# Kernel tuning notes

Measured on AMD Instinct MI355X. Metric: run time of the kernel, lower is better.

The kernel has to match this reference:

```python
import jax, jax.numpy as jnp
import numpy as np

EMBED_DIM = 512
N_HEADS = 8
HEAD_DIM = EMBED_DIM // N_HEADS


def setup_inputs() -> dict:
    key = jax.random.key(0)
    ks = jax.random.split(key, 8)
    B, S, D = 8, 2048, EMBED_DIM
    scale = 1.0 / np.sqrt(D)
    return {
        "key": jax.random.normal(ks[0], (B, S, D), dtype=jnp.float32),
        "query": jax.random.normal(ks[1], (B, S, D), dtype=jnp.float32),
        "value": jax.random.normal(ks[2], (B, S, D), dtype=jnp.float32),
        # nn.Linear stores weight as [out, in]; y = x @ W.T. We store W_T=[in,out].
        "Wq": jax.random.normal(ks[3], (D, D), dtype=jnp.float32) * scale,
        "Wk": jax.random.normal(ks[4], (D, D), dtype=jnp.float32) * scale,
        "Wv": jax.random.normal(ks[5], (D, D), dtype=jnp.float32) * scale,
        "Wo": jax.random.normal(ks[6], (D, D), dtype=jnp.float32) * scale,
        "bo": jax.random.normal(ks[7], (D,), dtype=jnp.float32) * scale,
    }


def reference(key, query, value, Wq, Wk, Wv, Wo, bo):
    B, S, D = key.shape
    Sq = query.shape[1]
    H, Hd = N_HEADS, HEAD_DIM
    # projections (no bias for q/k/v)
    q = (query @ Wq).reshape(B, Sq, H, Hd)
    k = (key @ Wk).reshape(B, S, H, Hd)
    v = (value @ Wv).reshape(B, S, H, Hd)
    # scores: [B, H, Sq, S]
    product = jnp.einsum("bqhd,bkhd->bhqk", q, k) / np.sqrt(Hd)
    scores = jax.nn.softmax(product, axis=-1)
    out = jnp.einsum("bhqk,bkhd->bqhd", scores, v).reshape(B, Sq, D)
    return out @ Wo + bo
```

## Files before the change

### kernel.cpp

```cpp
#include <hip/hip_runtime.h>

typedef _Float16 half8 __attribute__((ext_vector_type(8)));
typedef _Float16 half4 __attribute__((ext_vector_type(4)));
typedef __fp16 fp16x2 __attribute__((ext_vector_type(2)));
typedef float floatx16 __attribute__((ext_vector_type(16)));
typedef unsigned int uint2v __attribute__((ext_vector_type(2)));

#define MFMA_F16 __builtin_amdgcn_mfma_f32_32x32x16_f16

__device__ __forceinline__ float fast_exp2(float x) {
#if __has_builtin(__builtin_amdgcn_exp2f)
    return __builtin_amdgcn_exp2f(x);
#else
    return exp2f(x);
#endif
}

__device__ __forceinline__ half4 pack4(float a, float b, float c, float d) {
    union { fp16x2 p[2]; half4 h; } u;
    u.p[0] = __builtin_amdgcn_cvt_pkrtz(a, b);
    u.p[1] = __builtin_amdgcn_cvt_pkrtz(c, d);
    return u.h;
}

__device__ __forceinline__ unsigned int pk2(float a, float b) {
    union { fp16x2 p; unsigned int u; } v;
    v.p = __builtin_amdgcn_cvt_pkrtz(a, b);
    return v.u;
}

__device__ __forceinline__ half8 ld_frag_lds(const _Float16* p) {
    union { half8 v; half4 h[2]; } u;
    u.h[0] = *(const half4*)(p);
    u.h[1] = *(const half4*)(p + 4);
    return u.v;
}

__device__ __forceinline__ void tile_barrier() {
    asm volatile("s_waitcnt lgkmcnt(0)" ::: "memory");
    __builtin_amdgcn_s_barrier();
    asm volatile("" ::: "memory");
}

__device__ __forceinline__ half8 pv_frag(const unsigned int* w, int i0) {
    uint2v s0 = __builtin_amdgcn_permlane32_swap(w[2 * i0 + 0], w[2 * i0 + 2], false, false);
    uint2v s1 = __builtin_amdgcn_permlane32_swap(w[2 * i0 + 1], w[2 * i0 + 3], false, false);
    union { unsigned int u[4]; half8 h; } pu;
    pu.u[0] = s0[0];
    pu.u[1] = s1[0];
    pu.u[2] = s0[1];
    pu.u[3] = s1[1];
    return pu.h;
}

__global__ __launch_bounds__(256) void wcvt_kernel(const float* __restrict__ Wq,
                                                   const float* __restrict__ Wk,
                                                   const float* __restrict__ Wv,
                                                   const float* __restrict__ Wo,
                                                   _Float16* __restrict__ Wt) {
    __shared__ _Float16 T[64 * 68];
    const int bx   = blockIdx.x;
    const int wsel = bx >> 6;
    const int tile = bx & 63;
    const int to   = (tile >> 3) * 64;
    const int ti   = (tile & 7) * 64;
    const float* src = (wsel == 0) ? Wq : (wsel == 1) ? Wk : (wsel == 2) ? Wv : Wo;
    const int t = threadIdx.x;
    const int rloc = t >> 4, c4 = (t & 15) * 4;
#pragma unroll
    for (int m = 0; m < 4; m++) {
        int i = ti + rloc + 16 * m;
        float4 f = *(const float4*)(src + (size_t)i * 512 + to + c4);
        T[(c4 + 0) * 68 + rloc + 16 * m] = (_Float16)f.x;
        T[(c4 + 1) * 68 + rloc + 16 * m] = (_Float16)f.y;
        T[(c4 + 2) * 68 + rloc + 16 * m] = (_Float16)f.z;
        T[(c4 + 3) * 68 + rloc + 16 * m] = (_Float16)f.w;
    }
    __syncthreads();
    const int o_loc = t >> 2, ich = (t & 3) * 16;
    const _Float16* s = &T[o_loc * 68 + ich];
    _Float16* dst = Wt + (size_t)wsel * 262144 + (size_t)(to + o_loc) * 512 + ti + ich;
    half4 a0 = *(const half4*)(s);
    half4 a1 = *(const half4*)(s + 4);
    half4 a2 = *(const half4*)(s + 8);
    half4 a3 = *(const half4*)(s + 12);
    *(half4*)(dst)      = a0;
    *(half4*)(dst + 4)  = a1;
    *(half4*)(dst + 8)  = a2;
    *(half4*)(dst + 12) = a3;
}

__global__ __launch_bounds__(256, 3) void qkv_gemm(const float* __restrict__ query,
                                                   const float* __restrict__ key,
                                                   const float* __restrict__ value,
                                                   const _Float16* __restrict__ Wt,
                                                   _Float16* __restrict__ Qh,
                                                   _Float16* __restrict__ Kh,
                                                   _Float16* __restrict__ Vt,
                                                   float C1) {
    __shared__ _Float16 Alds[128 * 68];
    __shared__ _Float16 Blds[128 * 68];

    const int z = blockIdx.z;
    const float* A = (z == 0) ? query : (z == 1) ? key : value;
    const _Float16* W = Wt + (size_t)z * 262144;

    const int tid  = threadIdx.x;
    const int lane = tid & 63;
    const int w    = tid >> 6;
    const int l31  = lane & 31;
    const int lh   = lane >> 5;
    const int wm   = w >> 1;
    const int wn   = w & 1;
    const int n0   = blockIdx.x * 128;
    const int m0   = blockIdx.y * 128;
    const int crow = tid >> 3;
    const int ck8  = (tid & 7) * 8;

    floatx16 acc[2][2];
#pragma unroll
    for (int i = 0; i < 2; i++)
#pragma unroll
        for (int j = 0; j < 2; j++)
#pragma unroll
            for (int r = 0; r < 16; r++) acc[i][j][r] = 0.0f;

    float4 apre[4][2];
    int4   bpre[4];
#pragma unroll
    for (int i = 0; i < 4; i++) {
        const float* p = A + (size_t)(m0 + crow + 32 * i) * 512 + ck8;
        apre[i][0] = *(const float4*)(p);
        apre[i][1] = *(const float4*)(p + 4);
        bpre[i] = *(const int4*)(W + (size_t)(n0 + crow + 32 * i) * 512 + ck8);
    }

    for (int t = 0; t < 8; t++) {
        __syncthreads();
#pragma unroll
        for (int i = 0; i < 4; i++) {
            int r = crow + 32 * i;
            float4 f0 = apre[i][0], f1 = apre[i][1];
            *(half4*)&Alds[r * 68 + ck8]     = pack4(f0.x, f0.y, f0.z, f0.w);
            *(half4*)&Alds[r * 68 + ck8 + 4] = pack4(f1.x, f1.y, f1.z, f1.w);
            *(int2*)&Blds[r * 68 + ck8]      = make_int2(bpre[i].x, bpre[i].y);
            *(int2*)&Blds[r * 68 + ck8 + 4]  = make_int2(bpre[i].z, bpre[i].w);
        }
        __syncthreads();
        if (t < 7) {
            int ks2 = (t + 1) * 64;
#pragma unroll
            for (int i = 0; i < 4; i++) {
                const float* p = A + (size_t)(m0 + crow + 32 * i) * 512 + ks2 + ck8;
                apre[i][0] = *(const float4*)(p);
                apre[i][1] = *(const float4*)(p + 4);
                bpre[i] = *(const int4*)(W + (size_t)(n0 + crow + 32 * i) * 512 + ks2 + ck8);
            }
        }
#pragma unroll
        for (int kc = 0; kc < 4; kc++) {
            int kb = kc * 16 + lh * 8;
            half8 af[2], bf[2];
            af[0] = ld_frag_lds(&Alds[(wm * 64 + l31) * 68 + kb]);
            af[1] = ld_frag_lds(&Alds[(wm * 64 + 32 + l31) * 68 + kb]);
            bf[0] = ld_frag_lds(&Blds[(wn * 64 + l31) * 68 + kb]);
            bf[1] = ld_frag_lds(&Blds[(wn * 64 + 32 + l31) * 68 + kb]);
#pragma unroll
            for (int i = 0; i < 2; i++)
#pragma unroll
                for (int j = 0; j < 2; j++)
                    acc[i][j] = MFMA_F16(af[i], bf[j], acc[i][j], 0, 0, 0);
        }
    }

    const float oscale = (z == 0) ? C1 : 1.0f;
    _Float16* out01 = (z == 0) ? Qh : Kh;
#pragma unroll
    for (int i = 0; i < 2; i++) {
#pragma unroll
        for (int j = 0; j < 2; j++) {
            int gn    = n0 + wn * 64 + j * 32 + l31;
            int mbase = m0 + wm * 64 + i * 32 + 4 * lh;
            int h = gn >> 6, hd = gn & 63;
            if (z < 2) {
#pragma unroll
                for (int r = 0; r < 16; r++) {
                    int gm = mbase + (r & 3) + 8 * (r >> 2);
                    int b = gm >> 11, s = gm & 2047;
                    out01[(size_t)((b * 8 + h) * 2048 + s) * 64 + hd] =
                        (_Float16)(acc[i][j][r] * oscale);
                }
            } else {
#pragma unroll
                for (int g = 0; g < 4; g++) {
                    int gm = mbase + 8 * g;
                    int b = gm >> 11, s = gm & 2047;
                    *(half4*)&Vt[(size_t)((b * 8 + h) * 64 + hd) * 2048 + s] =
                        pack4(acc[i][j][4 * g + 0], acc[i][j][4 * g + 1],
                              acc[i][j][4 * g + 2], acc[i][j][4 * g + 3]);
                }
            }
        }
    }
}

__global__ __launch_bounds__(256, 3) void out_gemm(const _Float16* __restrict__ A,
                                                   const _Float16* __restrict__ W,
                                                   const float* __restrict__ bias,
                                                   float* __restrict__ out) {
    __shared__ _Float16 Alds[128 * 68];
    __shared__ _Float16 Blds[128 * 68];

    const int tid  = threadIdx.x;
    const int lane = tid & 63;
    const int w    = tid >> 6;
    const int l31  = lane & 31;
    const int lh   = lane >> 5;
    const int wm   = w >> 1;
    const int wn   = w & 1;
    const int n0   = blockIdx.x * 128;
    const int m0   = blockIdx.y * 128;
    const int crow = tid >> 3;
    const int ck8  = (tid & 7) * 8;

    floatx16 acc[2][2];
#pragma unroll
    for (int i = 0; i < 2; i++)
#pragma unroll
        for (int j = 0; j < 2; j++)
#pragma unroll
            for (int r = 0; r < 16; r++) acc[i][j][r] = 0.0f;

    int4 apre[4], bpre[4];
#pragma unroll
    for (int i = 0; i < 4; i++) {
        apre[i] = *(const int4*)(A + (size_t)(m0 + crow + 32 * i) * 512 + ck8);
        bpre[i] = *(const int4*)(W + (size_t)(n0 + crow + 32 * i) * 512 + ck8);
    }

    for (int t = 0; t < 8; t++) {
        __syncthreads();
#pragma unroll
        for (int i = 0; i < 4; i++) {
            int r = crow + 32 * i;
            *(int2*)&Alds[r * 68 + ck8]     = make_int2(apre[i].x, apre[i].y);
            *(int2*)&Alds[r * 68 + ck8 + 4] = make_int2(apre[i].z, apre[i].w);
            *(int2*)&Blds[r * 68 + ck8]     = make_int2(bpre[i].x, bpre[i].y);
            *(int2*)&Blds[r * 68 + ck8 + 4] = make_int2(bpre[i].z, bpre[i].w);
        }
        __syncthreads();
        if (t < 7) {
            int ks2 = (t + 1) * 64;
#pragma unroll
            for (int i = 0; i < 4; i++) {
                apre[i] = *(const int4*)(A + (size_t)(m0 + crow + 32 * i) * 512 + ks2 + ck8);
                bpre[i] = *(const int4*)(W + (size_t)(n0 + crow + 32 * i) * 512 + ks2 + ck8);
            }
        }
#pragma unroll
        for (int kc = 0; kc < 4; kc++) {
            int kb = kc * 16 + lh * 8;
            half8 af[2], bf[2];
            af[0] = ld_frag_lds(&Alds[(wm * 64 + l31) * 68 + kb]);
            af[1] = ld_frag_lds(&Alds[(wm * 64 + 32 + l31) * 68 + kb]);
            bf[0] = ld_frag_lds(&Blds[(wn * 64 + l31) * 68 + kb]);
            bf[1] = ld_frag_lds(&Blds[(wn * 64 + 32 + l31) * 68 + kb]);
#pragma unroll
            for (int i = 0; i < 2; i++)
#pragma unroll
                for (int j = 0; j < 2; j++)
                    acc[i][j] = MFMA_F16(af[i], bf[j], acc[i][j], 0, 0, 0);
        }
    }

#pragma unroll
    for (int i = 0; i < 2; i++) {
#pragma unroll
        for (int j = 0; j < 2; j++) {
            int gn    = n0 + wn * 64 + j * 32 + l31;
            int mbase = m0 + wm * 64 + i * 32 + 4 * lh;
            float bv = bias[gn];
#pragma unroll
            for (int r = 0; r < 16; r++) {
                int gm = mbase + (r & 3) + 8 * (r >> 2);
                out[(size_t)gm * 512 + gn] = acc[i][j][r] + bv;
            }
        }
    }
}

__global__ __launch_bounds__(256, 3) void attn_kernel(const _Float16* __restrict__ Qg,
                                                      const _Float16* __restrict__ Kg,
                                                      const _Float16* __restrict__ Vg,
                                                      _Float16* __restrict__ AO) {
    __shared__ _Float16 Kbuf[2][64 * 68];

    const int tid  = threadIdx.x;
    const int lane = tid & 63;
    const int w    = tid >> 6;
    const int l31  = lane & 31;
    const int lh   = lane >> 5;
    const int h    = blockIdx.y;
    const int b    = blockIdx.z;
    const int q0   = blockIdx.x * 128 + w * 32;

    const size_t bhoff = (size_t)(b * 8 + h) * (2048 * 64);
    const _Float16* Qbh = Qg + bhoff;
    const _Float16* Kbh = Kg + bhoff;
    const _Float16* Vbh = Vg + bhoff;

    const _Float16* Vrow0 = Vbh + (size_t)l31 * 2048 + lh * 8;
    const _Float16* Vrow1 = Vbh + (size_t)(32 + l31) * 2048 + lh * 8;

    const int c0row = tid >> 3, ck8 = (tid & 7) * 8;
    const int c1row = c0row + 32;

    half8 qf[4];
#pragma unroll
    for (int kc = 0; kc < 4; kc++)
        qf[kc] = *(const half8*)(Qbh + (size_t)(q0 + l31) * 64 + kc * 16 + lh * 8);

    floatx16 O[2];
#pragma unroll
    for (int i = 0; i < 2; i++)
#pragma unroll
        for (int r = 0; r < 16; r++) O[i][r] = 0.0f;
    float lsum = 0.0f;

    unsigned int w16[16];
    half8 vf[4][2];

    int4 kpre[2];
    kpre[0] = *(const int4*)(Kbh + c0row * 64 + ck8);
    kpre[1] = *(const int4*)(Kbh + c1row * 64 + ck8);
    *(int2*)&Kbuf[0][c0row * 68 + ck8]     = make_int2(kpre[0].x, kpre[0].y);
    *(int2*)&Kbuf[0][c0row * 68 + ck8 + 4] = make_int2(kpre[0].z, kpre[0].w);
    *(int2*)&Kbuf[0][c1row * 68 + ck8]     = make_int2(kpre[1].x, kpre[1].y);
    *(int2*)&Kbuf[0][c1row * 68 + ck8 + 4] = make_int2(kpre[1].z, kpre[1].w);
    kpre[0] = *(const int4*)(Kbh + 4096 + c0row * 64 + ck8);
    kpre[1] = *(const int4*)(Kbh + 4096 + c1row * 64 + ck8);
    tile_barrier();

    for (int kt = 0; kt < 32; kt++) {
        const int cur = kt & 1;
        const _Float16* Kc = Kbuf[cur];

#pragma unroll
        for (int kc = 0; kc < 4; kc++) {
            vf[kc][0] = *(const half8*)(Vrow0 + kt * 64 + kc * 16);
            vf[kc][1] = *(const half8*)(Vrow1 + kt * 64 + kc * 16);
        }

        if (kt < 31) {
            _Float16* Kd = Kbuf[cur ^ 1];
            *(int2*)&Kd[c0row * 68 + ck8]     = make_int2(kpre[0].x, kpre[0].y);
            *(int2*)&Kd[c0row * 68 + ck8 + 4] = make_int2(kpre[0].z, kpre[0].w);
            *(int2*)&Kd[c1row * 68 + ck8]     = make_int2(kpre[1].x, kpre[1].y);
            *(int2*)&Kd[c1row * 68 + ck8 + 4] = make_int2(kpre[1].z, kpre[1].w);
        }
        if (kt < 30) {
            const _Float16* Ksrc = Kbh + (size_t)(kt + 2) * 4096;
            kpre[0] = *(const int4*)(Ksrc + c0row * 64 + ck8);
            kpre[1] = *(const int4*)(Ksrc + c1row * 64 + ck8);
        }

        floatx16 Sf[2];
#pragma unroll
        for (int i = 0; i < 2; i++)
#pragma unroll
            for (int r = 0; r < 16; r++) Sf[i][r] = 0.0f;
#pragma unroll
        for (int kc = 0; kc < 4; kc++) {
#pragma unroll
            for (int ms = 0; ms < 2; ms++) {
                half8 kf = ld_frag_lds(&Kc[(ms * 32 + l31) * 68 + kc * 16 + lh * 8]);
                Sf[ms] = MFMA_F16(kf, qf[kc], Sf[ms], 0, 0, 0);
            }
        }

        float rsA = 0.0f, rsB = 0.0f;
#pragma unroll
        for (int i = 0; i < 8; i++) {
            int ms = i >> 2, g = i & 3;
            float p0 = fast_exp2(Sf[ms][4 * g + 0]);
            float p1 = fast_exp2(Sf[ms][4 * g + 1]);
            float p2 = fast_exp2(Sf[ms][4 * g + 2]);
            float p3 = fast_exp2(Sf[ms][4 * g + 3]);
            rsA += p0 + p1;
            rsB += p2 + p3;
            w16[2 * i + 0] = pk2(p0, p1);
            w16[2 * i + 1] = pk2(p2, p3);
        }
        lsum += rsA + rsB;

#pragma unroll
        for (int kc = 0; kc < 4; kc++) {
            int i0 = (kc >> 1) * 4 + (kc & 1) * 2;
            half8 pf = pv_frag(w16, i0);
            O[0] = MFMA_F16(vf[kc][0], pf, O[0], 0, 0, 0);
            O[1] = MFMA_F16(vf[kc][1], pf, O[1], 0, 0, 0);
        }

        tile_barrier();
    }

    lsum += __shfl_xor(lsum, 32);
    float inv = 1.0f / lsum;
    int q = q0 + l31;
#pragma unroll
    for (int hs = 0; hs < 2; hs++) {
#pragma unroll
        for (int g = 0; g < 4; g++) {
            *(half4*)&AO[(size_t)(b * 2048 + q) * 512 + h * 64 + hs * 32 + g * 8 + lh * 4] =
                pack4(O[hs][4 * g + 0] * inv, O[hs][4 * g + 1] * inv,
                      O[hs][4 * g + 2] * inv, O[hs][4 * g + 3] * inv);
        }
    }
}

extern "C" void kernel_launch(void* const* d_in, const int* in_sizes, int n_in,
                              void* d_out, int out_size, void* d_ws, size_t ws_size,
                              hipStream_t stream) {
    const float* key   = (const float*)d_in[0];
    const float* query = (const float*)d_in[1];
    const float* value = (const float*)d_in[2];
    const float* Wq    = (const float*)d_in[3];
    const float* Wk    = (const float*)d_in[4];
    const float* Wv    = (const float*)d_in[5];
    const float* Wo    = (const float*)d_in[6];
    const float* bo    = (const float*)d_in[7];

    _Float16* ws = (_Float16*)d_ws;
    _Float16* Wt = ws;
    _Float16* Qh = ws + 1048576;
    _Float16* Kh = Qh + 8388608;
    _Float16* Vt = Kh + 8388608;
    _Float16* AO = Vt + 8388608;

    const float C1 = 0.18033688011112042f;

    wcvt_kernel<<<dim3(256), dim3(256), 0, stream>>>(Wq, Wk, Wv, Wo, Wt);

    qkv_gemm<<<dim3(4, 128, 3), dim3(256), 0, stream>>>(query, key, value, Wt,
                                                        Qh, Kh, Vt, C1);

    attn_kernel<<<dim3(16, 8, 8), dim3(256), 0, stream>>>(Qh, Kh, Vt, AO);

    out_gemm<<<dim3(4, 128), dim3(256), 0, stream>>>(AO, Wt + 3 * 262144, bo,
                                                     (float*)d_out);
}
```

Before: 343.4 us.

## Stage V through LDS, widen key tile to 128, software-pipeline PV MFMAs

The attention kernel now processes 128 keys per iteration instead of 64. V tiles are double-buffered through shared memory with coalesced loads, where previously each lane read fragments directly from global memory. The P·V MFMAs of the previous tile are deferred into the next iteration so they overlap with the loads and QK^T of the current tile, and fewer barriers are needed. The cost is higher register and LDS use, so occupancy launch bounds drop from 3 to 2. The GEMM kernels also swap __syncthreads for tile_barrier.

```diff
diff --git a/kernel.cpp b/kernel.cpp
--- a/kernel.cpp
+++ b/kernel.cpp
@@ -136,7 +136,7 @@
     }
 
     for (int t = 0; t < 8; t++) {
-        __syncthreads();
+        tile_barrier();
 #pragma unroll
         for (int i = 0; i < 4; i++) {
             int r = crow + 32 * i;
@@ -146,7 +146,7 @@
             *(int2*)&Blds[r * 68 + ck8]      = make_int2(bpre[i].x, bpre[i].y);
             *(int2*)&Blds[r * 68 + ck8 + 4]  = make_int2(bpre[i].z, bpre[i].w);
         }
-        __syncthreads();
+        tile_barrier();
         if (t < 7) {
             int ks2 = (t + 1) * 64;
 #pragma unroll
@@ -239,7 +239,7 @@
     }
 
     for (int t = 0; t < 8; t++) {
-        __syncthreads();
+        tile_barrier();
 #pragma unroll
         for (int i = 0; i < 4; i++) {
             int r = crow + 32 * i;
@@ -248,7 +248,7 @@
             *(int2*)&Blds[r * 68 + ck8]     = make_int2(bpre[i].x, bpre[i].y);
             *(int2*)&Blds[r * 68 + ck8 + 4] = make_int2(bpre[i].z, bpre[i].w);
         }
-        __syncthreads();
+        tile_barrier();
         if (t < 7) {
             int ks2 = (t + 1) * 64;
 #pragma unroll
@@ -289,11 +289,12 @@
     }
 }
 
-__global__ __launch_bounds__(256, 3) void attn_kernel(const _Float16* __restrict__ Qg,
+__global__ __launch_bounds__(256, 2) void attn_kernel(const _Float16* __restrict__ Qg,
                                                       const _Float16* __restrict__ Kg,
                                                       const _Float16* __restrict__ Vg,
                                                       _Float16* __restrict__ AO) {
-    __shared__ _Float16 Kbuf[2][64 * 68];
+    __shared__ _Float16 Kbuf[2][128 * 68];
+    __shared__ _Float16 Vbuf[2][64 * 132];
 
     const int tid  = threadIdx.x;
     const int lane = tid & 63;
@@ -309,11 +310,8 @@
     const _Float16* Kbh = Kg + bhoff;
     const _Float16* Vbh = Vg + bhoff;
 
-    const _Float16* Vrow0 = Vbh + (size_t)l31 * 2048 + lh * 8;
-    const _Float16* Vrow1 = Vbh + (size_t)(32 + l31) * 2048 + lh * 8;
-
     const int c0row = tid >> 3, ck8 = (tid & 7) * 8;
-    const int c1row = c0row + 32;
+    const int vrow  = tid >> 2, vcol = (tid & 3) * 32;
 
     half8 qf[4];
 #pragma unroll
@@ -327,52 +325,89 @@
         for (int r = 0; r < 16; r++) O[i][r] = 0.0f;
     float lsum = 0.0f;
 
-    unsigned int w16[16];
-    half8 vf[4][2];
-
-    int4 kpre[2];
-    kpre[0] = *(const int4*)(Kbh + c0row * 64 + ck8);
-    kpre[1] = *(const int4*)(Kbh + c1row * 64 + ck8);
-    *(int2*)&Kbuf[0][c0row * 68 + ck8]     = make_int2(kpre[0].x, kpre[0].y);
-    *(int2*)&Kbuf[0][c0row * 68 + ck8 + 4] = make_int2(kpre[0].z, kpre[0].w);
-    *(int2*)&Kbuf[0][c1row * 68 + ck8]     = make_int2(kpre[1].x, kpre[1].y);
-    *(int2*)&Kbuf[0][c1row * 68 + ck8 + 4] = make_int2(kpre[1].z, kpre[1].w);
-    kpre[0] = *(const int4*)(Kbh + 4096 + c0row * 64 + ck8);
-    kpre[1] = *(const int4*)(Kbh + 4096 + c1row * 64 + ck8);
+    unsigned int w16[32];
+    half8 vf[8][2];
+
+    int4 kpre[4], vpre[4];
+#pragma unroll
+    for (int i = 0; i < 4; i++)
+        kpre[i] = *(const int4*)(Kbh + (size_t)(c0row + 32 * i) * 64 + ck8);
+#pragma unroll
+    for (int j = 0; j < 4; j++)
+        vpre[j] = *(const int4*)(Vbh + (size_t)vrow * 2048 + vcol + 8 * j);
+#pragma unroll
+    for (int i = 0; i < 4; i++) {
+        *(int2*)&Kbuf[0][(c0row + 32 * i) * 68 + ck8]     = make_int2(kpre[i].x, kpre[i].y);
+        *(int2*)&Kbuf[0][(c0row + 32 * i) * 68 + ck8 + 4] = make_int2(kpre[i].z, kpre[i].w);
+    }
+#pragma unroll
+    for (int j = 0; j < 4; j++) {
+        *(int2*)&Vbuf[0][vrow * 132 + vcol + 8 * j]     = make_int2(vpre[j].x, vpre[j].y);
+        *(int2*)&Vbuf[0][vrow * 132 + vcol + 8 * j + 4] = make_int2(vpre[j].z, vpre[j].w);
+    }
+#pragma unroll
+    for (int i = 0; i < 4; i++)
+        kpre[i] = *(const int4*)(Kbh + 8192 + (size_t)(c0row + 32 * i) * 64 + ck8);
+#pragma unroll
+    for (int j = 0; j < 4; j++)
+        vpre[j] = *(const int4*)(Vbh + 128 + (size_t)vrow * 2048 + vcol + 8 * j);
     tile_barrier();
 
-    for (int kt = 0; kt < 32; kt++) {
+    for (int kt = 0; kt < 16; kt++) {
         const int cur = kt & 1;
         const _Float16* Kc = Kbuf[cur];
-
+        const _Float16* Vc = Vbuf[cur];
+
+        if (kt > 0) {
+#pragma unroll
+            for (int kc = 0; kc < 8; kc++) {
+                int i0 = 2 * kc;
+                half8 pf = pv_frag(w16, i0);
+                O[0] = MFMA_F16(vf[kc][0], pf, O[0], 0, 0, 0);
+                O[1] = MFMA_F16(vf[kc][1], pf, O[1], 0, 0, 0);
+            }
+        }
+
+        if (kt < 15) {
+            _Float16* Kd = Kbuf[cur ^ 1];
+            _Float16* Vd = Vbuf[cur ^ 1];
+#pragma unroll
+            for (int i = 0; i < 4; i++) {
+                *(int2*)&Kd[(c0row + 32 * i) * 68 + ck8]     = make_int2(kpre[i].x, kpre[i].y);
+                *(int2*)&Kd[(c0row + 32 * i) * 68 + ck8 + 4] = make_int2(kpre[i].z, kpre[i].w);
+            }
+#pragma unroll
+            for (int j = 0; j < 4; j++) {
+                *(int2*)&Vd[vrow * 132 + vcol + 8 * j]     = make_int2(vpre[j].x, vpre[j].y);
+                *(int2*)&Vd[vrow * 132 + vcol + 8 * j + 4] = make_int2(vpre[j].z, vpre[j].w);
+            }
+        }
+        if (kt < 14) {
+            const _Float16* Ksrc = Kbh + (size_t)(kt + 2) * 8192;
+            const _Float16* Vsrc = Vbh + (size_t)(kt + 2) * 128;
+#pragma unroll
+            for (int i = 0; i < 4; i++)
+                kpre[i] = *(const int4*)(Ksrc + (size_t)(c0row + 32 * i) * 64 + ck8);
+#pragma unroll
+            for (int j = 0; j < 4; j++)
+                vpre[j] = *(const int4*)(Vsrc + (size_t)vrow * 2048 + vcol + 8 * j);
+        }
+
+#pragma unroll
+        for (int kc = 0; kc < 8; kc++) {
+            vf[kc][0] = ld_frag_lds(&Vc[(l31)*132      + kc * 16 + lh * 8]);
+            vf[kc][1] = ld_frag_lds(&Vc[(32 + l31)*132 + kc * 16 + lh * 8]);
+        }
+
+        floatx16 Sf[4];
+#pragma unroll
+        for (int i = 0; i < 4; i++)
+#pragma unroll
+            for (int r = 0; r < 16; r++) Sf[i][r] = 0.0f;
 #pragma unroll
         for (int kc = 0; kc < 4; kc++) {
-            vf[kc][0] = *(const half8*)(Vrow0 + kt * 64 + kc * 16);
-            vf[kc][1] = *(const half8*)(Vrow1 + kt * 64 + kc * 16);
-        }
-
-        if (kt < 31) {
-            _Float16* Kd = Kbuf[cur ^ 1];
-            *(int2*)&Kd[c0row * 68 + ck8]     = make_int2(kpre[0].x, kpre[0].y);
-            *(int2*)&Kd[c0row * 68 + ck8 + 4] = make_int2(kpre[0].z, kpre[0].w);
-            *(int2*)&Kd[c1row * 68 + ck8]     = make_int2(kpre[1].x, kpre[1].y);
-            *(int2*)&Kd[c1row * 68 + ck8 + 4] = make_int2(kpre[1].z, kpre[1].w);
-        }
-        if (kt < 30) {
-            const _Float16* Ksrc = Kbh + (size_t)(kt + 2) * 4096;
-            kpre[0] = *(const int4*)(Ksrc + c0row * 64 + ck8);
-            kpre[1] = *(const int4*)(Ksrc + c1row * 64 + ck8);
-        }
-
-        floatx16 Sf[2];
-#pragma unroll
-        for (int i = 0; i < 2; i++)
-#pragma unroll
-            for (int r = 0; r < 16; r++) Sf[i][r] = 0.0f;
-#pragma unroll
-        for (int kc = 0; kc < 4; kc++) {
-#pragma unroll
-            for (int ms = 0; ms < 2; ms++) {
+#pragma unroll
+            for (int ms = 0; ms < 4; ms++) {
                 half8 kf = ld_frag_lds(&Kc[(ms * 32 + l31) * 68 + kc * 16 + lh * 8]);
                 Sf[ms] = MFMA_F16(kf, qf[kc], Sf[ms], 0, 0, 0);
             }
@@ -380,7 +415,7 @@
 
         float rsA = 0.0f, rsB = 0.0f;
 #pragma unroll
-        for (int i = 0; i < 8; i++) {
+        for (int i = 0; i < 16; i++) {
             int ms = i >> 2, g = i & 3;
             float p0 = fast_exp2(Sf[ms][4 * g + 0]);
             float p1 = fast_exp2(Sf[ms][4 * g + 1]);
@@ -393,15 +428,15 @@
         }
         lsum += rsA + rsB;
 
-#pragma unroll
-        for (int kc = 0; kc < 4; kc++) {
-            int i0 = (kc >> 1) * 4 + (kc & 1) * 2;
-            half8 pf = pv_frag(w16, i0);
-            O[0] = MFMA_F16(vf[kc][0], pf, O[0], 0, 0, 0);
-            O[1] = MFMA_F16(vf[kc][1], pf, O[1], 0, 0, 0);
-        }
-
         tile_barrier();
+    }
+
+#pragma unroll
+    for (int kc = 0; kc < 8; kc++) {
+        int i0 = 2 * kc;
+        half8 pf = pv_frag(w16, i0);
+        O[0] = MFMA_F16(vf[kc][0], pf, O[0], 0, 0, 0);
+        O[1] = MFMA_F16(vf[kc][1], pf, O[1], 0, 0, 0);
     }
 
     lsum += __shfl_xor(lsum, 32);
```

Measured after the change: 298.5 us. -13.1%, faster.
